# Performance work log

Measured on AMD Instinct MI355X. Metric: run time of the kernel, lower is better.

## Reference

```python
import jax, jax.numpy as jnp
import numpy as np

# config
B, V, S, D = 2, 8, 256, 2048
NH, NKV, KVR = 32, 8, 2
HD = D // NH            # 64
G = NH // NKV           # GQA group size = 4
INIT = 0.02


def _neighbor_idx():
    # replicates generate_neighbor: left neighbors (i-half..i-1) then right (i+1..i+half), circular
    half = KVR // 2
    offsets = np.concatenate([np.arange(-half, 0), np.arange(1, half + 1)])
    return (np.arange(V)[:, None] + offsets[None, :]) % V  # [V, KVR]


def setup_inputs() -> dict:
    key = jax.random.key(0)
    k1, k2, k3, k4 = jax.random.split(key, 4)
    x = jax.random.normal(k1, (B, V, S, D), jnp.float32)
    wq = jax.random.normal(k2, (D, NH * HD), jnp.float32) * INIT
    wkv = jax.random.normal(k3, (D, 2 * NKV * HD), jnp.float32) * INIT
    wo = jax.random.normal(k4, (D, D), jnp.float32) * INIT
    return {"x": x, "wq": wq, "wkv": wkv, "wo": wo}


def reference(x, wq, wkv, wo):
    b, v, s, d = x.shape
    idx = _neighbor_idx()  # [V, KVR] static

    # Q projection: [b, v, s, NH*HD]
    xq = (x @ wq).reshape(b, v, s, NKV, G, HD)  # grouped-query layout (kv head, group)

    # neighbor gather: [b, v, KVR, s, d] -> [b, v, KVR*s, d]
    x_kv = x[:, idx].reshape(b, v, KVR * s, d)
    kv = x_kv @ wkv
    xk, xv = jnp.split(kv, 2, axis=-1)
    xk = xk.reshape(b, v, KVR * s, NKV, HD)
    xv = xv.reshape(b, v, KVR * s, NKV, HD)

    # grouped-query SDPA (no mask, eval mode): avoids materializing repeated K/V
    scale = 1.0 / jnp.sqrt(jnp.asarray(HD, x.dtype))
    scores = jnp.einsum('bvsngh,bvtnh->bvngst', xq, xk) * scale  # [b,v,NKV,G,s,KVR*s]
    attn = jax.nn.softmax(scores, axis=-1)
    out = jnp.einsum('bvngst,bvtnh->bvsngh', attn, xv).reshape(b, v, s, d)
    return out @ wo
```

## Files before the change

### kernel.cpp

```cpp
#include <hip/hip_runtime.h>
#include <stdint.h>

typedef unsigned short u16;
typedef unsigned int   u32;
typedef short short8 __attribute__((ext_vector_type(8)));
typedef float f32x4  __attribute__((ext_vector_type(4)));

__device__ __forceinline__ u16 f2bf(float f){
  u32 u = __builtin_bit_cast(u32, f);
  u32 r = (u + 0x7FFFu + ((u >> 16) & 1u)) >> 16;
  return (u16)r;
}
__device__ __forceinline__ u32 cvtpk(float a, float b){
  u32 r; asm("v_cvt_pk_bf16_f32 %0, %1, %2" : "=v"(r) : "v"(a), "v"(b)); return r;
}
__device__ __forceinline__ void gload16(const u16* g, u16* l){
  __builtin_amdgcn_global_load_lds((const __attribute__((address_space(1))) void*)g,
                                   (__attribute__((address_space(3))) void*)l, 16, 0, 0);
}
#define BARRIER()  do{ __builtin_amdgcn_s_barrier(); __builtin_amdgcn_sched_barrier(0); }while(0)

__global__ __launch_bounds__(256) void k_cvt_bf16(const float* __restrict__ x,
                                                  u16* __restrict__ y, int n8){
  int i = blockIdx.x * 256 + threadIdx.x;
  if (i >= n8) return;
  const float4* p = (const float4*)x + (size_t)i * 2;
  float4 a = p[0], b = p[1];
  short8 o;
  o[0] = f2bf(a.x); o[1] = f2bf(a.y); o[2] = f2bf(a.z); o[3] = f2bf(a.w);
  o[4] = f2bf(b.x); o[5] = f2bf(b.y); o[6] = f2bf(b.z); o[7] = f2bf(b.w);
  *(short8*)(y + (size_t)i * 8) = o;
}

__global__ __launch_bounds__(256) void k_transpose_w(const float* __restrict__ in,
                                                     u16* __restrict__ out, int R, int C){
  __shared__ float tile[32][33];
  int nc = C >> 5;
  int cb = blockIdx.x % nc, rb = blockIdx.x / nc;
  int tx = threadIdx.x & 31, ty = threadIdx.x >> 5;
#pragma unroll
  for (int i = 0; i < 4; ++i){
    int r = rb * 32 + ty + i * 8;
    tile[ty + i * 8][tx] = in[(size_t)r * C + cb * 32 + tx];
  }
  __syncthreads();
#pragma unroll
  for (int i = 0; i < 4; ++i){
    int c = cb * 32 + ty + i * 8;
    out[(size_t)c * R + rb * 32 + tx] = f2bf(tile[tx][ty + i * 8]);
  }
}

template<int BM, int BN, int MH, int NFRAG, int ALOADS, int BLOADS, bool QSCALE, typename CT>
__global__ __launch_bounds__(512) void k_gemm8p(const u16* __restrict__ A,
                                                const u16* __restrict__ Bt,
                                                CT* __restrict__ C,
                                                int N, int K){
  constexpr int SZA = BM * 128;
  constexpr int SZB = BN * 128;
  constexpr int SZ  = SZA + SZB;
  constexpr int WTM = BM / 2;
  constexpr int WTN = BN / 4;
  __shared__ char lds[2 * SZ];

  int tid = threadIdx.x, lane = tid & 63, wid = tid >> 6;
  int l16 = lane & 15, g4 = lane >> 4;
  int wm = wid >> 2, wn = wid & 3;
  int bid = blockIdx.x;
  int cpx = (int)gridDim.x >> 3;
  int wg = (bid & 7) * cpx + (bid >> 3);
  int nb = N / BN;
  int bm = wg / nb, bn = wg % nb;

  const u16* baseA = A  + (size_t)(bm * BM) * K;
  const u16* baseB = Bt + (size_t)(bn * BN) * K;

  int aLds[ALOADS], aG[ALOADS];
#pragma unroll
  for (int i = 0; i < ALOADS; ++i){
    int q = (wid * ALOADS + i) * 1024 + lane * 16;
    int row = q >> 7, c = q & 127;
    int cs = c ^ ((row & 7) << 4);
    aLds[i] = q; aG[i] = row * K + (cs >> 1);
  }
  int bLds[BLOADS], bG[BLOADS];
#pragma unroll
  for (int j = 0; j < BLOADS; ++j){
    int q = (wid * BLOADS + j) * 1024 + lane * 16;
    int row = q >> 7, c = q & 127;
    int cs = c ^ ((row & 7) << 4);
    bLds[j] = q; bG[j] = row * K + (cs >> 1);
  }
  auto stageA = [&](int t){
    char* dst = lds + (t & 1) * SZ;
#pragma unroll
    for (int i = 0; i < ALOADS; ++i) gload16(baseA + aG[i] + t * 64, (u16*)(dst + aLds[i]));
  };
  auto stageB = [&](int t){
    char* dst = lds + (t & 1) * SZ + SZA;
#pragma unroll
    for (int j = 0; j < BLOADS; ++j) gload16(baseB + bG[j] + t * 64, (u16*)(dst + bLds[j]));
  };
  auto rdA = [&](const char* Ab, int m, int ks){
    int row = wm * WTM + m * 16 + l16;
    return *(const short8*)(Ab + row * 128 + ((ks * 64 + g4 * 16) ^ ((row & 7) << 4)));
  };
  auto rdB = [&](const char* Bb, int nf, int ks){
    int row = wn * WTN + nf * 16 + l16;
    return *(const short8*)(Bb + row * 128 + ((ks * 64 + g4 * 16) ^ ((row & 7) << 4)));
  };

  f32x4 zero4 = {0.f, 0.f, 0.f, 0.f};
  f32x4 acc[2 * MH][NFRAG];
#pragma unroll
  for (int i = 0; i < 2 * MH; ++i)
#pragma unroll
    for (int j = 0; j < NFRAG; ++j) acc[i][j] = zero4;

  int NK = K >> 6;
  stageA(0); stageB(0);
  asm volatile("s_waitcnt vmcnt(0)" ::: "memory");
  BARRIER();
  short8 a0[MH], a1[MH], a2[MH], a3[MH], bf0[NFRAG], bf1[NFRAG];
#pragma unroll
  for (int nf = 0; nf < NFRAG; ++nf) bf0[nf] = rdB(lds + SZA, nf, 0);
#pragma unroll
  for (int m = 0; m < MH; ++m)       a0[m]  = rdA(lds, m, 0);

  for (int kt = 0; kt < NK; ++kt){
    const char* Ab = lds + (kt & 1) * SZ;
    const char* Bb = Ab + SZA;
    bool st = (kt + 1 < NK);
#pragma unroll
    for (int m = 0; m < MH; ++m) a1[m] = rdA(Ab, MH + m, 0);
    if (st) stageA(kt + 1);
    BARRIER();
    __builtin_amdgcn_s_setprio(1);
#pragma unroll
    for (int m = 0; m < MH; ++m)
#pragma unroll
      for (int nf = 0; nf < NFRAG; ++nf)
        acc[m][nf] = __builtin_amdgcn_mfma_f32_16x16x32_bf16(a0[m], bf0[nf], acc[m][nf], 0, 0, 0);
    __builtin_amdgcn_s_setprio(0);
#pragma unroll
    for (int nf = 0; nf < NFRAG; ++nf) bf1[nf] = rdB(Bb, nf, 1);
#pragma unroll
    for (int m = 0; m < MH; ++m)       a2[m]  = rdA(Ab, m, 1);
    if (st) stageB(kt + 1);
    BARRIER();
    __builtin_amdgcn_s_setprio(1);
#pragma unroll
    for (int m = 0; m < MH; ++m)
#pragma unroll
      for (int nf = 0; nf < NFRAG; ++nf)
        acc[MH + m][nf] = __builtin_amdgcn_mfma_f32_16x16x32_bf16(a1[m], bf0[nf], acc[MH + m][nf], 0, 0, 0);
    __builtin_amdgcn_s_setprio(0);
#pragma unroll
    for (int m = 0; m < MH; ++m) a3[m] = rdA(Ab, MH + m, 1);
    BARRIER();
    __builtin_amdgcn_s_setprio(1);
#pragma unroll
    for (int m = 0; m < MH; ++m)
#pragma unroll
      for (int nf = 0; nf < NFRAG; ++nf)
        acc[m][nf] = __builtin_amdgcn_mfma_f32_16x16x32_bf16(a2[m], bf1[nf], acc[m][nf], 0, 0, 0);
    __builtin_amdgcn_s_setprio(0);
    if (st) asm volatile("s_waitcnt vmcnt(0)" ::: "memory");
    BARRIER();
    if (st){
      const char* Ab2 = lds + ((kt + 1) & 1) * SZ;
      const char* Bb2 = Ab2 + SZA;
#pragma unroll
      for (int nf = 0; nf < NFRAG; ++nf) bf0[nf] = rdB(Bb2, nf, 0);
#pragma unroll
      for (int m = 0; m < MH; ++m)       a0[m]  = rdA(Ab2, m, 0);
    }
    __builtin_amdgcn_s_setprio(1);
#pragma unroll
    for (int m = 0; m < MH; ++m)
#pragma unroll
      for (int nf = 0; nf < NFRAG; ++nf)
        acc[MH + m][nf] = __builtin_amdgcn_mfma_f32_16x16x32_bf16(a3[m], bf1[nf], acc[MH + m][nf], 0, 0, 0);
    __builtin_amdgcn_s_setprio(0);
    BARRIER();
  }

#pragma unroll
  for (int mf = 0; mf < 2 * MH; ++mf)
#pragma unroll
    for (int nf = 0; nf < NFRAG; ++nf)
#pragma unroll
      for (int r = 0; r < 4; ++r){
        int row = bm * BM + wm * WTM + mf * 16 + g4 * 4 + r;
        int col = bn * BN + wn * WTN + nf * 16 + l16;
        float vv = acc[mf][nf][r];
        if constexpr (QSCALE) { if (col < 2048) vv *= 0.18033688011112042f; }
        if constexpr (sizeof(CT) == 2) C[(size_t)row * N + col] = (CT)f2bf(vv);
        else                           C[(size_t)row * N + col] = (CT)vv;
      }
}

__global__ __launch_bounds__(256) void k_vt(const u16* __restrict__ c1, u16* __restrict__ vt){
  __shared__ u16 tile[64][72];
  int bid = blockIdx.x;
  int st = bid & 3, n = (bid >> 2) & 7, bv = bid >> 5;
  int t = threadIdx.x;
  int sr = t >> 2, sc = t & 3;
  const u16* src = c1 + (size_t)(bv * 256 + st * 64 + sr) * 3072 + 2560 + n * 64 + sc * 16;
  short8 a = *(const short8*)src;
  short8 b = *(const short8*)(src + 8);
  *(short8*)&tile[sr][sc * 16]     = a;
  *(short8*)&tile[sr][sc * 16 + 8] = b;
  __syncthreads();
  int h = t >> 2, c2 = t & 3;
  short8 o0, o1;
#pragma unroll
  for (int j = 0; j < 8; ++j) o0[j] = (short)tile[c2 * 16 + j][h];
#pragma unroll
  for (int j = 0; j < 8; ++j) o1[j] = (short)tile[c2 * 16 + 8 + j][h];
  u16* dst = vt + (size_t)((bv * 8 + n) * 64 + h) * 256 + st * 64 + c2 * 16;
  *(short8*)dst       = o0;
  *(short8*)(dst + 8) = o1;
}

__global__ __launch_bounds__(256, 2) void k_attn(const u16* __restrict__ c1,
                                                 const u16* __restrict__ vt,
                                                 u16* __restrict__ att){
  __shared__ u16 Klds[64][72];
  __shared__ u16 Vlds[64][72];
  __shared__ u16 Plds[4][16][72];
  int bid = blockIdx.x;
  int qt = bid & 3, n = (bid >> 2) & 7, v = (bid >> 5) & 7, b = bid >> 8;
  int tid = threadIdx.x;
  int g = tid >> 6, lane = tid & 63, l16 = lane & 15, g4 = lane >> 4;
  int bv = b * 8 + v;
  int rowQ = bv * 256 + qt * 64;
  int qcol = n * 256 + g * 64;

  short8 qf[4][2];
#pragma unroll
  for (int qi = 0; qi < 4; ++qi)
#pragma unroll
    for (int kk = 0; kk < 2; ++kk)
      qf[qi][kk] = *(const short8*)(c1 + (size_t)(rowQ + qi * 16 + l16) * 3072
                                     + qcol + kk * 32 + g4 * 8);

  f32x4 zero4 = {0.f, 0.f, 0.f, 0.f};
  f32x4 O[4][4];
#pragma unroll
  for (int i = 0; i < 4; ++i)
#pragma unroll
    for (int j = 0; j < 4; ++j) O[i][j] = zero4;
  float m2[4]   = {-3.0e38f, -3.0e38f, -3.0e38f, -3.0e38f};
  float lsum[4] = {0.f, 0.f, 0.f, 0.f};

  int sr = tid >> 2, sc = tid & 3;
  short8 k0, k1, v0, v1;
  {
    int vn = (v + 7) & 7;
    const u16* ks = c1 + (size_t)((b * 8 + vn) * 256 + sr) * 3072 + 2048 + n * 64 + sc * 16;
    k0 = *(const short8*)ks; k1 = *(const short8*)(ks + 8);
    const u16* vs = vt + (size_t)(((b * 8 + vn) * 8 + n) * 64 + sr) * 256 + sc * 16;
    v0 = *(const short8*)vs; v1 = *(const short8*)(vs + 8);
  }

  for (int ti = 0; ti < 8; ++ti){
    __syncthreads();
    *(short8*)&Klds[sr][sc * 16]     = k0;
    *(short8*)&Klds[sr][sc * 16 + 8] = k1;
    *(short8*)&Vlds[sr][sc * 16]     = v0;
    *(short8*)&Vlds[sr][sc * 16 + 8] = v1;
    __syncthreads();
    if (ti < 7){
      int tn = ti + 1;
      int vn = (tn < 4) ? ((v + 7) & 7) : ((v + 1) & 7);
      int tb = (tn & 3) * 64;
      const u16* ks = c1 + (size_t)((b * 8 + vn) * 256 + tb + sr) * 3072 + 2048 + n * 64 + sc * 16;
      k0 = *(const short8*)ks; k1 = *(const short8*)(ks + 8);
      const u16* vs = vt + (size_t)(((b * 8 + vn) * 8 + n) * 64 + sr) * 256 + tb + sc * 16;
      v0 = *(const short8*)vs; v1 = *(const short8*)(vs + 8);
    }
    short8 kf[4][2], vf[2][4];
#pragma unroll
    for (int kt = 0; kt < 4; ++kt)
#pragma unroll
      for (int ks = 0; ks < 2; ++ks)
        kf[kt][ks] = *(const short8*)&Klds[kt * 16 + l16][ks * 32 + g4 * 8];
#pragma unroll
    for (int ks = 0; ks < 2; ++ks)
#pragma unroll
      for (int hi = 0; hi < 4; ++hi)
        vf[ks][hi] = *(const short8*)&Vlds[hi * 16 + l16][ks * 32 + g4 * 8];

#pragma unroll
    for (int qi = 0; qi < 4; ++qi){
      f32x4 sa[4];
#pragma unroll
      for (int kt = 0; kt < 4; ++kt){
        sa[kt] = zero4;
#pragma unroll
        for (int ks = 0; ks < 2; ++ks)
          sa[kt] = __builtin_amdgcn_mfma_f32_16x16x32_bf16(kf[kt][ks], qf[qi][ks], sa[kt], 0, 0, 0);
      }
      float pmax = sa[0][0];
#pragma unroll
      for (int kt = 0; kt < 4; ++kt)
#pragma unroll
        for (int r = 0; r < 4; ++r) pmax = fmaxf(pmax, sa[kt][r]);
      pmax = fmaxf(pmax, __shfl_xor(pmax, 16));
      pmax = fmaxf(pmax, __shfl_xor(pmax, 32));
      if (__any(pmax > m2[qi] + 8.f)){
        float mnew  = fmaxf(m2[qi], pmax);
        float alpha = exp2f(m2[qi] - mnew);
        m2[qi] = mnew;
        lsum[qi] *= alpha;
        float ab[4];
#pragma unroll
        for (int r = 0; r < 4; ++r) ab[r] = __shfl(alpha, g4 * 4 + r);
#pragma unroll
        for (int hi = 0; hi < 4; ++hi)
#pragma unroll
          for (int r = 0; r < 4; ++r) O[qi][hi][r] *= ab[r];
      }
      float m = m2[qi];
      float psum = 0.f;
      u32 w[4][2];
#pragma unroll
      for (int kt = 0; kt < 4; ++kt){
        float p0 = exp2f(sa[kt][0] - m);
        float p1 = exp2f(sa[kt][1] - m);
        float p2 = exp2f(sa[kt][2] - m);
        float p3 = exp2f(sa[kt][3] - m);
        psum += (p0 + p1) + (p2 + p3);
        w[kt][0] = cvtpk(p0, p1);
        w[kt][1] = cvtpk(p2, p3);
      }
      psum += __shfl_xor(psum, 16);
      psum += __shfl_xor(psum, 32);
      lsum[qi] += psum;
      u32* prow = (u32*)&Plds[g][l16][0];
#pragma unroll
      for (int kt = 0; kt < 4; ++kt){
        prow[kt * 8 + g4 * 2]     = w[kt][0];
        prow[kt * 8 + g4 * 2 + 1] = w[kt][1];
      }
      short8 pa[2];
#pragma unroll
      for (int ks = 0; ks < 2; ++ks)
        pa[ks] = *(const short8*)&Plds[g][l16][ks * 32 + g4 * 8];
#pragma unroll
      for (int hi = 0; hi < 4; ++hi)
#pragma unroll
        for (int ks = 0; ks < 2; ++ks)
          O[qi][hi] = __builtin_amdgcn_mfma_f32_16x16x32_bf16(pa[ks], vf[ks][hi], O[qi][hi], 0, 0, 0);
    }
  }
#pragma unroll
  for (int qi = 0; qi < 4; ++qi){
    float lb[4];
#pragma unroll
    for (int r = 0; r < 4; ++r) lb[r] = 1.0f / __shfl(lsum[qi], g4 * 4 + r);
#pragma unroll
    for (int hi = 0; hi < 4; ++hi)
#pragma unroll
      for (int r = 0; r < 4; ++r){
        int row = rowQ + qi * 16 + g4 * 4 + r;
        int col = qcol + hi * 16 + l16;
        att[(size_t)row * 2048 + col] = f2bf(O[qi][hi][r] * lb[r]);
      }
  }
}

extern "C" void kernel_launch(void* const* d_in, const int* in_sizes, int n_in,
                              void* d_out, int out_size, void* d_ws, size_t ws_size,
                              hipStream_t stream){
  const float* x   = (const float*)d_in[0];
  const float* wq  = (const float*)d_in[1];
  const float* wkv = (const float*)d_in[2];
  const float* wo  = (const float*)d_in[3];
  float* out = (float*)d_out;
  char* ws = (char*)d_ws;

  u16* x_bf  = (u16*)(ws);
  u16* wqkvt = (u16*)(ws + 16777216);
  u16* wot   = (u16*)(ws + 29360128);
  u16* c1    = (u16*)(ws + 37748736);
  u16* vt    = (u16*)(ws + 62914560);
  u16* att   = x_bf;

  k_cvt_bf16<<<4096, 256, 0, stream>>>(x, x_bf, 1048576);
  k_transpose_w<<<4096, 256, 0, stream>>>(wq,  wqkvt,               2048, 2048);
  k_transpose_w<<<2048, 256, 0, stream>>>(wkv, wqkvt + 2048 * 2048, 2048, 1024);
  k_transpose_w<<<4096, 256, 0, stream>>>(wo,  wot,                 2048, 2048);
  k_gemm8p<128, 192, 2, 3, 2, 3, true,  u16  ><<<512, 512, 0, stream>>>(x_bf, wqkvt, c1, 3072, 2048);
  k_vt<<<512, 256, 0, stream>>>(c1, vt);
  k_attn<<<512, 256, 0, stream>>>(c1, vt, att);
  k_gemm8p<128, 128, 2, 2, 2, 2, false, float><<<512, 512, 0, stream>>>(att, wot, out, 2048, 2048);
}
```

Measured before the change: 153.9 us.

## Replace 8-wave GEMM with 4-wave triple-buffered K=32 pipeline

Swaps the 512-thread double-buffered GEMM (K-tile 64) for a 256-thread kernel with three LDS stages of K-tile 32. Loads are issued two steps ahead, and partial vmcnt waits replace full drains. Tile shapes also change: QKV uses 256x96 and the output projection uses 128x128 with 4 waves, so each wave holds more accumulators. This aims to hide global-load latency and cut barriers per FLOP, at the cost of higher register pressure, fewer waves per block, and dummy B loads into a padding area when B slices do not cover all waves.

```diff
diff --git a/kernel.cpp b/kernel.cpp
--- a/kernel.cpp
+++ b/kernel.cpp
@@ -51,21 +51,22 @@
   }
 }
 
-template<int BM, int BN, int MH, int NFRAG, int ALOADS, int BLOADS, bool QSCALE, typename CT>
-__global__ __launch_bounds__(512) void k_gemm8p(const u16* __restrict__ A,
+template<int BM, int BN, int NF, bool QSCALE, typename CT>
+__global__ __launch_bounds__(256) void k_gemm4w(const u16* __restrict__ A,
                                                 const u16* __restrict__ Bt,
                                                 CT* __restrict__ C,
                                                 int N, int K){
-  constexpr int SZA = BM * 128;
-  constexpr int SZB = BN * 128;
-  constexpr int SZ  = SZA + SZB;
-  constexpr int WTM = BM / 2;
-  constexpr int WTN = BN / 4;
-  __shared__ char lds[2 * SZ];
+  constexpr int MFR     = BM / 32;
+  constexpr int MHALF   = MFR / 2;
+  constexpr int ALOADS  = BM / 64;
+  constexpr int BSLICES = BN / 16;
+  constexpr int TL      = ALOADS + 2;
+  constexpr int SZ      = (BM + BN) * 64;
+  __shared__ char lds[3 * SZ + 1024];
 
   int tid = threadIdx.x, lane = tid & 63, wid = tid >> 6;
   int l16 = lane & 15, g4 = lane >> 4;
-  int wm = wid >> 2, wn = wid & 3;
+  int wm = wid >> 1, wn = wid & 1;
   int bid = blockIdx.x;
   int cpx = (int)gridDim.x >> 3;
   int wg = (bid & 7) * cpx + (bid >> 3);
@@ -79,120 +80,108 @@
 #pragma unroll
   for (int i = 0; i < ALOADS; ++i){
     int q = (wid * ALOADS + i) * 1024 + lane * 16;
-    int row = q >> 7, c = q & 127;
-    int cs = c ^ ((row & 7) << 4);
+    int row = q >> 6, c = q & 63;
+    int cs = c ^ ((row & 3) << 4);
     aLds[i] = q; aG[i] = row * K + (cs >> 1);
   }
-  int bLds[BLOADS], bG[BLOADS];
-#pragma unroll
-  for (int j = 0; j < BLOADS; ++j){
-    int q = (wid * BLOADS + j) * 1024 + lane * 16;
-    int row = q >> 7, c = q & 127;
-    int cs = c ^ ((row & 7) << 4);
-    bLds[j] = q; bG[j] = row * K + (cs >> 1);
-  }
-  auto stageA = [&](int t){
-    char* dst = lds + (t & 1) * SZ;
-#pragma unroll
-    for (int i = 0; i < ALOADS; ++i) gload16(baseA + aG[i] + t * 64, (u16*)(dst + aLds[i]));
+  int bLds[2], bG[2]; bool bOk[2];
+#pragma unroll
+  for (int j = 0; j < 2; ++j){
+    int slice = wid + j * 4;
+    bOk[j] = (slice < BSLICES);
+    int s = bOk[j] ? slice : 0;
+    int q = s * 1024 + lane * 16;
+    int row = q >> 6, c = q & 63;
+    int cs = c ^ ((row & 3) << 4);
+    bLds[j] = bOk[j] ? (BM * 64 + q) : (3 * SZ + lane * 16);
+    bG[j] = row * K + (cs >> 1);
+  }
+  auto stage = [&](int t){
+    char* dst = lds + (t % 3) * SZ;
+#pragma unroll
+    for (int i = 0; i < ALOADS; ++i) gload16(baseA + aG[i] + t * 32, (u16*)(dst + aLds[i]));
+#pragma unroll
+    for (int j = 0; j < 2; ++j){
+      char* d = bOk[j] ? (dst + bLds[j]) : (lds + bLds[j]);
+      gload16(baseB + bG[j] + t * 32, (u16*)d);
+    }
   };
-  auto stageB = [&](int t){
-    char* dst = lds + (t & 1) * SZ + SZA;
-#pragma unroll
-    for (int j = 0; j < BLOADS; ++j) gload16(baseB + bG[j] + t * 64, (u16*)(dst + bLds[j]));
+  auto rdA = [&](int buf, int m){
+    int row = wm * (BM / 2) + m * 16 + l16;
+    return *(const short8*)(lds + buf * SZ + row * 64 + ((g4 * 16) ^ ((row & 3) << 4)));
   };
-  auto rdA = [&](const char* Ab, int m, int ks){
-    int row = wm * WTM + m * 16 + l16;
-    return *(const short8*)(Ab + row * 128 + ((ks * 64 + g4 * 16) ^ ((row & 7) << 4)));
+  auto rdB = [&](int buf, int nf){
+    int row = wn * (NF * 16) + nf * 16 + l16;
+    return *(const short8*)(lds + buf * SZ + BM * 64 + row * 64 + ((g4 * 16) ^ ((row & 3) << 4)));
   };
-  auto rdB = [&](const char* Bb, int nf, int ks){
-    int row = wn * WTN + nf * 16 + l16;
-    return *(const short8*)(Bb + row * 128 + ((ks * 64 + g4 * 16) ^ ((row & 7) << 4)));
-  };
 
   f32x4 zero4 = {0.f, 0.f, 0.f, 0.f};
-  f32x4 acc[2 * MH][NFRAG];
-#pragma unroll
-  for (int i = 0; i < 2 * MH; ++i)
-#pragma unroll
-    for (int j = 0; j < NFRAG; ++j) acc[i][j] = zero4;
-
-  int NK = K >> 6;
-  stageA(0); stageB(0);
-  asm volatile("s_waitcnt vmcnt(0)" ::: "memory");
+  f32x4 acc[MFR][NF];
+#pragma unroll
+  for (int i = 0; i < MFR; ++i)
+#pragma unroll
+    for (int j = 0; j < NF; ++j) acc[i][j] = zero4;
+
+  short8 aP[MHALF], aN[MHALF], bf[NF], bfN[NF];
+
+  int NK = K >> 5;
+  stage(0); stage(1);
+  if constexpr (TL == 6) asm volatile("s_waitcnt vmcnt(6)" ::: "memory");
+  else                   asm volatile("s_waitcnt vmcnt(4)" ::: "memory");
   BARRIER();
-  short8 a0[MH], a1[MH], a2[MH], a3[MH], bf0[NFRAG], bf1[NFRAG];
-#pragma unroll
-  for (int nf = 0; nf < NFRAG; ++nf) bf0[nf] = rdB(lds + SZA, nf, 0);
-#pragma unroll
-  for (int m = 0; m < MH; ++m)       a0[m]  = rdA(lds, m, 0);
+#pragma unroll
+  for (int m = 0; m < MHALF; ++m) aP[m] = rdA(0, m);
+#pragma unroll
+  for (int f = 0; f < NF; ++f)    bf[f] = rdB(0, f);
 
   for (int kt = 0; kt < NK; ++kt){
-    const char* Ab = lds + (kt & 1) * SZ;
-    const char* Bb = Ab + SZA;
-    bool st = (kt + 1 < NK);
-#pragma unroll
-    for (int m = 0; m < MH; ++m) a1[m] = rdA(Ab, MH + m, 0);
-    if (st) stageA(kt + 1);
+    int bcur = kt % 3;
     BARRIER();
+    if (kt + 2 < NK) stage(kt + 2);
+#pragma unroll
+    for (int m = 0; m < MHALF; ++m) aN[m] = rdA(bcur, MHALF + m);
     __builtin_amdgcn_s_setprio(1);
 #pragma unroll
-    for (int m = 0; m < MH; ++m)
-#pragma unroll
-      for (int nf = 0; nf < NFRAG; ++nf)
-        acc[m][nf] = __builtin_amdgcn_mfma_f32_16x16x32_bf16(a0[m], bf0[nf], acc[m][nf], 0, 0, 0);
+    for (int m = 0; m < MHALF; ++m)
+#pragma unroll
+      for (int f = 0; f < NF; ++f)
+        acc[m][f] = __builtin_amdgcn_mfma_f32_16x16x32_bf16(aP[m], bf[f], acc[m][f], 0, 0, 0);
     __builtin_amdgcn_s_setprio(0);
-#pragma unroll
-    for (int nf = 0; nf < NFRAG; ++nf) bf1[nf] = rdB(Bb, nf, 1);
-#pragma unroll
-    for (int m = 0; m < MH; ++m)       a2[m]  = rdA(Ab, m, 1);
-    if (st) stageB(kt + 1);
-    BARRIER();
+    if (kt + 1 < NK){
+      if (kt + 2 < NK){
+        if constexpr (TL == 6) asm volatile("s_waitcnt vmcnt(6)" ::: "memory");
+        else                   asm volatile("s_waitcnt vmcnt(4)" ::: "memory");
+      } else {
+        asm volatile("s_waitcnt vmcnt(0)" ::: "memory");
+      }
+      BARRIER();
+      int bnext = (kt + 1) % 3;
+#pragma unroll
+      for (int m = 0; m < MHALF; ++m) aP[m] = rdA(bnext, m);
+#pragma unroll
+      for (int f = 0; f < NF; ++f)    bfN[f] = rdB(bnext, f);
+    }
     __builtin_amdgcn_s_setprio(1);
 #pragma unroll
-    for (int m = 0; m < MH; ++m)
-#pragma unroll
-      for (int nf = 0; nf < NFRAG; ++nf)
-        acc[MH + m][nf] = __builtin_amdgcn_mfma_f32_16x16x32_bf16(a1[m], bf0[nf], acc[MH + m][nf], 0, 0, 0);
+    for (int m = 0; m < MHALF; ++m)
+#pragma unroll
+      for (int f = 0; f < NF; ++f)
+        acc[MHALF + m][f] = __builtin_amdgcn_mfma_f32_16x16x32_bf16(aN[m], bf[f], acc[MHALF + m][f], 0, 0, 0);
     __builtin_amdgcn_s_setprio(0);
-#pragma unroll
-    for (int m = 0; m < MH; ++m) a3[m] = rdA(Ab, MH + m, 1);
-    BARRIER();
-    __builtin_amdgcn_s_setprio(1);
-#pragma unroll
-    for (int m = 0; m < MH; ++m)
-#pragma unroll
-      for (int nf = 0; nf < NFRAG; ++nf)
-        acc[m][nf] = __builtin_amdgcn_mfma_f32_16x16x32_bf16(a2[m], bf1[nf], acc[m][nf], 0, 0, 0);
-    __builtin_amdgcn_s_setprio(0);
-    if (st) asm volatile("s_waitcnt vmcnt(0)" ::: "memory");
-    BARRIER();
-    if (st){
-      const char* Ab2 = lds + ((kt + 1) & 1) * SZ;
-      const char* Bb2 = Ab2 + SZA;
-#pragma unroll
-      for (int nf = 0; nf < NFRAG; ++nf) bf0[nf] = rdB(Bb2, nf, 0);
-#pragma unroll
-      for (int m = 0; m < MH; ++m)       a0[m]  = rdA(Ab2, m, 0);
-    }
-    __builtin_amdgcn_s_setprio(1);
-#pragma unroll
-    for (int m = 0; m < MH; ++m)
-#pragma unroll
-      for (int nf = 0; nf < NFRAG; ++nf)
-        acc[MH + m][nf] = __builtin_amdgcn_mfma_f32_16x16x32_bf16(a3[m], bf1[nf], acc[MH + m][nf], 0, 0, 0);
-    __builtin_amdgcn_s_setprio(0);
-    BARRIER();
-  }
-
-#pragma unroll
-  for (int mf = 0; mf < 2 * MH; ++mf)
-#pragma unroll
-    for (int nf = 0; nf < NFRAG; ++nf)
+    if (kt + 1 < NK){
+#pragma unroll
+      for (int f = 0; f < NF; ++f) bf[f] = bfN[f];
+    }
+  }
+
+#pragma unroll
+  for (int mf = 0; mf < MFR; ++mf)
+#pragma unroll
+    for (int nf = 0; nf < NF; ++nf)
 #pragma unroll
       for (int r = 0; r < 4; ++r){
-        int row = bm * BM + wm * WTM + mf * 16 + g4 * 4 + r;
-        int col = bn * BN + wn * WTN + nf * 16 + l16;
+        int row = bm * BM + wm * (BM / 2) + mf * 16 + g4 * 4 + r;
+        int col = bn * BN + wn * (NF * 16) + nf * 16 + l16;
         float vv = acc[mf][nf][r];
         if constexpr (QSCALE) { if (col < 2048) vv *= 0.18033688011112042f; }
         if constexpr (sizeof(CT) == 2) C[(size_t)row * N + col] = (CT)f2bf(vv);
@@ -392,8 +381,8 @@
   k_transpose_w<<<4096, 256, 0, stream>>>(wq,  wqkvt,               2048, 2048);
   k_transpose_w<<<2048, 256, 0, stream>>>(wkv, wqkvt + 2048 * 2048, 2048, 1024);
   k_transpose_w<<<4096, 256, 0, stream>>>(wo,  wot,                 2048, 2048);
-  k_gemm8p<128, 192, 2, 3, 2, 3, true,  u16  ><<<512, 512, 0, stream>>>(x_bf, wqkvt, c1, 3072, 2048);
+  k_gemm4w<256, 96, 3, true,  u16  ><<<512, 256, 0, stream>>>(x_bf, wqkvt, c1, 3072, 2048);
   k_vt<<<512, 256, 0, stream>>>(c1, vt);
   k_attn<<<512, 256, 0, stream>>>(c1, vt, att);
-  k_gemm8p<128, 128, 2, 2, 2, 2, false, float><<<512, 512, 0, stream>>>(att, wot, out, 2048, 2048);
-}
+  k_gemm4w<128, 128, 4, false, float><<<512, 256, 0, stream>>>(att, wot, out, 2048, 2048);
+}
```

New measurement: 170.0 us. +10.5%, slower.

## Fuse prep kernels into one launch and double-buffer attention K/V via direct-to-LDS loads

Applied to the files above, without the earlier changes.

The separate x conversion and three weight transpose launches are merged into one k_prep kernel that dispatches on block index, removing launch gaps. The attention kernel now double-buffers K/V tiles in LDS using global_load_lds with an XOR swizzle, so the next tile loads while the current one is computed, replacing the register-staged copy and its two barriers per iteration. This costs more LDS per block, which may lower occupancy, and relies on the swizzled layout keeping bank conflicts low.

```diff
diff --git a/kernel.cpp b/kernel.cpp
--- a/kernel.cpp
+++ b/kernel.cpp
@@ -20,24 +20,11 @@
 }
 #define BARRIER()  do{ __builtin_amdgcn_s_barrier(); __builtin_amdgcn_sched_barrier(0); }while(0)
 
-__global__ __launch_bounds__(256) void k_cvt_bf16(const float* __restrict__ x,
-                                                  u16* __restrict__ y, int n8){
-  int i = blockIdx.x * 256 + threadIdx.x;
-  if (i >= n8) return;
-  const float4* p = (const float4*)x + (size_t)i * 2;
-  float4 a = p[0], b = p[1];
-  short8 o;
-  o[0] = f2bf(a.x); o[1] = f2bf(a.y); o[2] = f2bf(a.z); o[3] = f2bf(a.w);
-  o[4] = f2bf(b.x); o[5] = f2bf(b.y); o[6] = f2bf(b.z); o[7] = f2bf(b.w);
-  *(short8*)(y + (size_t)i * 8) = o;
-}
-
-__global__ __launch_bounds__(256) void k_transpose_w(const float* __restrict__ in,
-                                                     u16* __restrict__ out, int R, int C){
-  __shared__ float tile[32][33];
+__device__ __forceinline__ void dev_transpose(const float* __restrict__ in,
+                                              u16* __restrict__ out, int R, int C,
+                                              int bid, int tx, int ty, float (*tile)[33]){
   int nc = C >> 5;
-  int cb = blockIdx.x % nc, rb = blockIdx.x / nc;
-  int tx = threadIdx.x & 31, ty = threadIdx.x >> 5;
+  int cb = bid % nc, rb = bid / nc;
 #pragma unroll
   for (int i = 0; i < 4; ++i){
     int r = rb * 32 + ty + i * 8;
@@ -49,6 +36,31 @@
     int c = cb * 32 + ty + i * 8;
     out[(size_t)c * R + rb * 32 + tx] = f2bf(tile[tx][ty + i * 8]);
   }
+}
+
+__global__ __launch_bounds__(256) void k_prep(const float* __restrict__ x,
+                                              const float* __restrict__ wq,
+                                              const float* __restrict__ wkv,
+                                              const float* __restrict__ wo,
+                                              u16* __restrict__ x_bf,
+                                              u16* __restrict__ wqkvt,
+                                              u16* __restrict__ wot){
+  __shared__ float tile[32][33];
+  int bid = blockIdx.x;
+  if (bid < 4096){
+    int i = bid * 256 + threadIdx.x;
+    const float4* p = (const float4*)x + (size_t)i * 2;
+    float4 a = p[0], b = p[1];
+    short8 o;
+    o[0] = f2bf(a.x); o[1] = f2bf(a.y); o[2] = f2bf(a.z); o[3] = f2bf(a.w);
+    o[4] = f2bf(b.x); o[5] = f2bf(b.y); o[6] = f2bf(b.z); o[7] = f2bf(b.w);
+    *(short8*)(x_bf + (size_t)i * 8) = o;
+    return;
+  }
+  int tx = threadIdx.x & 31, ty = threadIdx.x >> 5;
+  if (bid < 8192)       dev_transpose(wq,  wqkvt,               2048, 2048, bid - 4096,  tx, ty, tile);
+  else if (bid < 10240) dev_transpose(wkv, wqkvt + 2048 * 2048, 2048, 1024, bid - 8192,  tx, ty, tile);
+  else                  dev_transpose(wo,  wot,                 2048, 2048, bid - 10240, tx, ty, tile);
 }
 
 template<int BM, int BN, int MH, int NFRAG, int ALOADS, int BLOADS, bool QSCALE, typename CT>
@@ -226,8 +238,7 @@
 __global__ __launch_bounds__(256, 2) void k_attn(const u16* __restrict__ c1,
                                                  const u16* __restrict__ vt,
                                                  u16* __restrict__ att){
-  __shared__ u16 Klds[64][72];
-  __shared__ u16 Vlds[64][72];
+  __shared__ char KV[2][16384];
   __shared__ u16 Plds[4][16][72];
   int bid = blockIdx.x;
   int qt = bid & 3, n = (bid >> 2) & 7, v = (bid >> 5) & 7, b = bid >> 8;
@@ -237,6 +248,34 @@
   int rowQ = bv * 256 + qt * 64;
   int qcol = n * 256 + g * 64;
 
+  int srow[2], scol[2], qo[2];
+#pragma unroll
+  for (int i = 0; i < 2; ++i){
+    int q = i * 4096 + tid * 16;
+    int row = q >> 7, c = q & 127;
+    int cs = c ^ ((row & 7) << 4);
+    srow[i] = row; scol[i] = cs >> 1; qo[i] = q;
+  }
+  auto stage = [&](int t, int buf){
+    int vn = (t < 4) ? ((v + 7) & 7) : ((v + 1) & 7);
+    int tb = (t & 3) * 64;
+    const u16* kb = c1 + (size_t)((b * 8 + vn) * 256 + tb) * 3072 + 2048 + n * 64;
+    const u16* vb = vt + (size_t)(((b * 8 + vn) * 8 + n) * 64) * 256 + tb;
+    char* d = KV[buf];
+#pragma unroll
+    for (int i = 0; i < 2; ++i) gload16(kb + (size_t)srow[i] * 3072 + scol[i], (u16*)(d + qo[i]));
+#pragma unroll
+    for (int i = 0; i < 2; ++i) gload16(vb + (size_t)srow[i] * 256 + scol[i], (u16*)(d + 8192 + qo[i]));
+  };
+  auto rdK = [&](int buf, int kt, int ks){
+    int row = kt * 16 + l16;
+    return *(const short8*)(KV[buf] + row * 128 + ((ks * 64 + g4 * 16) ^ ((row & 7) << 4)));
+  };
+  auto rdV = [&](int buf, int hi, int ks){
+    int row = hi * 16 + l16;
+    return *(const short8*)(KV[buf] + 8192 + row * 128 + ((ks * 64 + g4 * 16) ^ ((row & 7) << 4)));
+  };
+
   short8 qf[4][2];
 #pragma unroll
   for (int qi = 0; qi < 4; ++qi)
@@ -254,43 +293,23 @@
   float m2[4]   = {-3.0e38f, -3.0e38f, -3.0e38f, -3.0e38f};
   float lsum[4] = {0.f, 0.f, 0.f, 0.f};
 
-  int sr = tid >> 2, sc = tid & 3;
-  short8 k0, k1, v0, v1;
-  {
-    int vn = (v + 7) & 7;
-    const u16* ks = c1 + (size_t)((b * 8 + vn) * 256 + sr) * 3072 + 2048 + n * 64 + sc * 16;
-    k0 = *(const short8*)ks; k1 = *(const short8*)(ks + 8);
-    const u16* vs = vt + (size_t)(((b * 8 + vn) * 8 + n) * 64 + sr) * 256 + sc * 16;
-    v0 = *(const short8*)vs; v1 = *(const short8*)(vs + 8);
-  }
+  stage(0, 0);
+  __syncthreads();
 
   for (int ti = 0; ti < 8; ++ti){
-    __syncthreads();
-    *(short8*)&Klds[sr][sc * 16]     = k0;
-    *(short8*)&Klds[sr][sc * 16 + 8] = k1;
-    *(short8*)&Vlds[sr][sc * 16]     = v0;
-    *(short8*)&Vlds[sr][sc * 16 + 8] = v1;
-    __syncthreads();
-    if (ti < 7){
-      int tn = ti + 1;
-      int vn = (tn < 4) ? ((v + 7) & 7) : ((v + 1) & 7);
-      int tb = (tn & 3) * 64;
-      const u16* ks = c1 + (size_t)((b * 8 + vn) * 256 + tb + sr) * 3072 + 2048 + n * 64 + sc * 16;
-      k0 = *(const short8*)ks; k1 = *(const short8*)(ks + 8);
-      const u16* vs = vt + (size_t)(((b * 8 + vn) * 8 + n) * 64 + sr) * 256 + tb + sc * 16;
-      v0 = *(const short8*)vs; v1 = *(const short8*)(vs + 8);
-    }
+    int buf = ti & 1;
+    if (ti < 7) stage(ti + 1, buf ^ 1);
     short8 kf[4][2], vf[2][4];
 #pragma unroll
     for (int kt = 0; kt < 4; ++kt)
 #pragma unroll
       for (int ks = 0; ks < 2; ++ks)
-        kf[kt][ks] = *(const short8*)&Klds[kt * 16 + l16][ks * 32 + g4 * 8];
+        kf[kt][ks] = rdK(buf, kt, ks);
 #pragma unroll
     for (int ks = 0; ks < 2; ++ks)
 #pragma unroll
       for (int hi = 0; hi < 4; ++hi)
-        vf[ks][hi] = *(const short8*)&Vlds[hi * 16 + l16][ks * 32 + g4 * 8];
+        vf[ks][hi] = rdV(buf, hi, ks);
 
 #pragma unroll
     for (int qi = 0; qi < 4; ++qi){
@@ -354,6 +373,7 @@
         for (int ks = 0; ks < 2; ++ks)
           O[qi][hi] = __builtin_amdgcn_mfma_f32_16x16x32_bf16(pa[ks], vf[ks][hi], O[qi][hi], 0, 0, 0);
     }
+    __syncthreads();
   }
 #pragma unroll
   for (int qi = 0; qi < 4; ++qi){
@@ -388,10 +408,7 @@
   u16* vt    = (u16*)(ws + 62914560);
   u16* att   = x_bf;
 
-  k_cvt_bf16<<<4096, 256, 0, stream>>>(x, x_bf, 1048576);
-  k_transpose_w<<<4096, 256, 0, stream>>>(wq,  wqkvt,               2048, 2048);
-  k_transpose_w<<<2048, 256, 0, stream>>>(wkv, wqkvt + 2048 * 2048, 2048, 1024);
-  k_transpose_w<<<4096, 256, 0, stream>>>(wo,  wot,                 2048, 2048);
+  k_prep<<<14336, 256, 0, stream>>>(x, wq, wkv, wo, x_bf, wqkvt, wot);
   k_gemm8p<128, 192, 2, 3, 2, 3, true,  u16  ><<<512, 512, 0, stream>>>(x_bf, wqkvt, c1, 3072, 2048);
   k_vt<<<512, 256, 0, stream>>>(c1, vt);
   k_attn<<<512, 256, 0, stream>>>(c1, vt, att);
```

Result: faster. 150.3 us (-2.4%).
